# Kernel optimization log

Hardware: AMD Instinct MI355X
Metric: run time of the kernel (lower is better)

## Reference

```python
import jax, jax.numpy as jnp
import numpy as np

N_NODES = 100000
IN_FEAT = 128
HIDDEN = 256
OUT = 2
N_EDGES = 600000
EPS = 1e-12  # F.normalize eps


def glorot(key, shape):
    fan_in, fan_out = shape[1], shape[0]
    lim = jnp.sqrt(6.0 / (fan_in + fan_out))
    return jax.random.uniform(key, shape, jnp.float32, -lim, lim)


def setup_inputs() -> dict:
    key = jax.random.key(0)
    ks = jax.random.split(key, 8)
    x = jax.random.normal(ks[0], (N_NODES, IN_FEAT), jnp.float32)
    edge_index = jax.random.randint(ks[1], (2, N_EDGES), 0, N_NODES, jnp.int64)
    return {
        'x': x,
        'edge_index': edge_index,
        'W1_l': glorot(ks[2], (HIDDEN, IN_FEAT)),
        'b1': jnp.zeros((HIDDEN,), jnp.float32),
        'W1_r': glorot(ks[3], (HIDDEN, IN_FEAT)),
        'W2_l': glorot(ks[4], (OUT, HIDDEN)),
        'b2': jnp.zeros((OUT,), jnp.float32),
        'W2_r': glorot(ks[5], (OUT, HIDDEN)),
    }


def sage_conv(x, src, dst, W_l, b_l, W_r):
    # mean aggregation of neighbor (source) features onto destination nodes
    msgs = x[src]  # [E, d]
    s = jax.ops.segment_sum(msgs, dst, num_segments=N_NODES)
    cnt = jax.ops.segment_sum(jnp.ones((src.shape[0], 1), x.dtype), dst,
                              num_segments=N_NODES)
    agg = s / jnp.maximum(cnt, 1.0)  # nodes with no in-edges stay 0
    out = agg @ W_l.T + b_l + x @ W_r.T  # lin_l(agg) + lin_r(x)
    # L2 normalize (normalize=True in SAGEConv)
    nrm = jnp.linalg.norm(out, axis=-1, keepdims=True)
    return out / jnp.maximum(nrm, EPS)


def reference(x, edge_index, W1_l, b1, W1_r, W2_l, b2, W2_r):
    src, dst = edge_index[0], edge_index[1]
    h = sage_conv(x, src, dst, W1_l, b1, W1_r)
    h = jax.nn.relu(h)
    # dropout(p=0.2) is identity in eval mode
    h = sage_conv(h, src, dst, W2_l, b2, W2_r)
    return jax.nn.log_softmax(h, axis=1)
```

## Files before the change

kernel.cpp:

```cpp
#include <hip/hip_runtime.h>
#include <hip/hip_fp16.h>

#define NN  100000
#define FIN 128
#define HID 256
#define NE  600000
#define FEPS 1e-12f


typedef _Float16 f16x8 __attribute__((ext_vector_type(8)));
typedef float    f32x4 __attribute__((ext_vector_type(4)));

__device__ __forceinline__ int clampN(int v) {
    return ((unsigned)v < (unsigned)NN) ? v : 0;
}
__device__ __forceinline__ int detect4(const int* ei) {
    return ((ei[1] | ei[3] | ei[5] | ei[7]) == 0) ? 1 : 0;
}
__device__ __forceinline__ int ld_src(const int* ei, int e, int f) {
    return f ? ei[2 * e] : ei[e];
}
__device__ __forceinline__ int ld_dst(const int* ei, int e, int f) {
    return f ? ei[2 * (NE + e)] : ei[NE + e];
}

__device__ __forceinline__ size_t fragIdx(int j, int k) {
    return ((size_t)((k >> 5) * 16 + (j >> 4)) * 64 +
            (size_t)(((k >> 3) & 3) * 16 + (j & 15))) * 8 + (k & 7);
}

__global__ __launch_bounds__(256) void setup_kernel(
    const int* __restrict__ ei,
    const float* __restrict__ x,
    const float* __restrict__ W1l, const float* __restrict__ W1r,
    __half* __restrict__ Bfh, __half* __restrict__ Bfl,
    __half* __restrict__ xh,
    int* __restrict__ cnt, int ncv)
{
    int b = blockIdx.x;
    int t = threadIdx.x;
    if (b < 256) {
        int j = b, k2 = t;
        float v = (k2 < FIN) ? W1l[(size_t)j * FIN + k2]
                             : W1r[(size_t)j * FIN + (k2 - FIN)];
        __half h  = __float2half_rn(v);
        __half lo = __float2half_rn(v - __half2float(h));
        size_t fi = fragIdx(j, k2);
        Bfh[fi] = h;
        Bfl[fi] = lo;
    } else if (b < 256 + ncv) {
        int idx = (b - 256) * 256 + t;
        if (idx < NN * FIN / 8) {
            const float4* px = (const float4*)(x + (size_t)idx * 8);
            float4 v0 = px[0], v1 = px[1];
            __half2 h0 = __float22half2_rn(make_float2(v0.x, v0.y));
            __half2 h1 = __float22half2_rn(make_float2(v0.z, v0.w));
            __half2 h2 = __float22half2_rn(make_float2(v1.x, v1.y));
            __half2 h3 = __float22half2_rn(make_float2(v1.z, v1.w));
            uint4 u;
            u.x = __builtin_bit_cast(unsigned, h0);
            u.y = __builtin_bit_cast(unsigned, h1);
            u.z = __builtin_bit_cast(unsigned, h2);
            u.w = __builtin_bit_cast(unsigned, h3);
            ((uint4*)xh)[idx] = u;
        }
    } else {
        int e = (b - 256 - ncv) * 256 + t;
        if (e < NE) {
            int f = detect4(ei);
            atomicAdd(cnt + clampN(ld_dst(ei, e, f)), 1);
        }
    }
}

__global__ __launch_bounds__(1024) void scan_a_kernel(
    const int* __restrict__ cnt, int* __restrict__ off, int* __restrict__ bsum)
{
    __shared__ int sm[1024];
    int t = threadIdx.x;
    int idx = blockIdx.x * 1024 + t;
    int v = (idx < NN) ? cnt[idx] : 0;
    sm[t] = v;
    __syncthreads();
    for (int d = 1; d < 1024; d <<= 1) {
        int w = (t >= d) ? sm[t - d] : 0;
        __syncthreads();
        sm[t] += w;
        __syncthreads();
    }
    if (idx < NN) off[idx] = sm[t] - v;
    if (t == 1023) bsum[blockIdx.x] = sm[1023];
}
__global__ __launch_bounds__(128) void scan_b_kernel(
    int* __restrict__ bsum, int* __restrict__ off, int nblocks)
{
    __shared__ int sm[128];
    int t = threadIdx.x;
    int v = (t < nblocks) ? bsum[t] : 0;
    sm[t] = v;
    __syncthreads();
    for (int d = 1; d < 128; d <<= 1) {
        int w = (t >= d) ? sm[t - d] : 0;
        __syncthreads();
        sm[t] += w;
        __syncthreads();
    }
    if (t < nblocks) bsum[t] = sm[t] - v;
    if (t == 0) off[NN] = NE;
}
__global__ __launch_bounds__(1024) void scan_c_kernel(
    const int* __restrict__ bsum, int* __restrict__ off)
{
    int idx = blockIdx.x * 1024 + threadIdx.x;
    if (idx < NN) off[idx] += bsum[blockIdx.x];
}

__global__ __launch_bounds__(256) void fill_kernel(
    const int* __restrict__ ei,
    const int* __restrict__ off, int* __restrict__ cur, int* __restrict__ col)
{
    int e = blockIdx.x * 256 + threadIdx.x;
    if (e >= NE) return;
    int f = detect4(ei);
    int src = clampN(ld_src(ei, e, f));
    int dst = clampN(ld_dst(ei, e, f));
    int p = atomicAdd(cur + dst, 1);
    col[off[dst] + p] = src;
}

__global__ __launch_bounds__(256) void gather_kernel(
    const int* __restrict__ off, const int* __restrict__ col,
    const __half* __restrict__ xh, float* __restrict__ agg)
{
    int idx = blockIdx.x * 256 + threadIdx.x;
    if (idx >= NN * 16) return;
    int n     = idx >> 4;
    int ft    = idx & 15;
    int fbase = ft * 8;

    float a[8];
#pragma unroll
    for (int i = 0; i < 8; ++i) a[i] = 0.0f;

    int s0 = off[n], s1 = off[n + 1];
    int i = s0;
    for (; i + 3 < s1; i += 4) {
        int c0 = clampN(col[i]);
        int c1 = clampN(col[i + 1]);
        int c2 = clampN(col[i + 2]);
        int c3 = clampN(col[i + 3]);
        uint4 v0 = *(const uint4*)(xh + (size_t)c0 * FIN + fbase);
        uint4 v1 = *(const uint4*)(xh + (size_t)c1 * FIN + fbase);
        uint4 v2 = *(const uint4*)(xh + (size_t)c2 * FIN + fbase);
        uint4 v3 = *(const uint4*)(xh + (size_t)c3 * FIN + fbase);
#pragma unroll
        for (int u = 0; u < 4; ++u) {
            float2 f0 = __half22float2(__builtin_bit_cast(__half2, (&v0.x)[u]));
            float2 f1 = __half22float2(__builtin_bit_cast(__half2, (&v1.x)[u]));
            float2 f2 = __half22float2(__builtin_bit_cast(__half2, (&v2.x)[u]));
            float2 f3 = __half22float2(__builtin_bit_cast(__half2, (&v3.x)[u]));
            a[2 * u]     += (f0.x + f1.x) + (f2.x + f3.x);
            a[2 * u + 1] += (f0.y + f1.y) + (f2.y + f3.y);
        }
    }
    for (; i < s1; ++i) {
        int c0 = clampN(col[i]);
        uint4 v0 = *(const uint4*)(xh + (size_t)c0 * FIN + fbase);
#pragma unroll
        for (int u = 0; u < 4; ++u) {
            float2 f0 = __half22float2(__builtin_bit_cast(__half2, (&v0.x)[u]));
            a[2 * u]     += f0.x;
            a[2 * u + 1] += f0.y;
        }
    }
    float ic = 1.0f / fmaxf((float)(s1 - s0), 1.0f);
    float4* dst = (float4*)(agg + (size_t)n * FIN + fbase);
    dst[0] = make_float4(a[0] * ic, a[1] * ic, a[2] * ic, a[3] * ic);
    dst[1] = make_float4(a[4] * ic, a[5] * ic, a[6] * ic, a[7] * ic);
}

__device__ __forceinline__ void storeHiLo4(
    __half* Ah, __half* Al, int row, int k, float4 v)
{
    int addr = row * 256 + ((((k >> 3) ^ (row & 7)) << 3) | (k & 7));
    __half h0 = __float2half_rn(v.x), h1 = __float2half_rn(v.y);
    __half h2 = __float2half_rn(v.z), h3 = __float2half_rn(v.w);
    __half l0 = __float2half_rn(v.x - __half2float(h0));
    __half l1 = __float2half_rn(v.y - __half2float(h1));
    __half l2 = __float2half_rn(v.z - __half2float(h2));
    __half l3 = __float2half_rn(v.w - __half2float(h3));
    uint2 uh, ul;
    uh.x = __builtin_bit_cast(unsigned, __halves2half2(h0, h1));
    uh.y = __builtin_bit_cast(unsigned, __halves2half2(h2, h3));
    ul.x = __builtin_bit_cast(unsigned, __halves2half2(l0, l1));
    ul.y = __builtin_bit_cast(unsigned, __halves2half2(l2, l3));
    *(uint2*)(Ah + addr) = uh;
    *(uint2*)(Al + addr) = ul;
}

__global__ __launch_bounds__(512, 4) void gemm_mfma_kernel(
    const float* __restrict__ agg, const float* __restrict__ x,
    const __half* __restrict__ Bfh, const __half* __restrict__ Bfl,
    const float* __restrict__ b1,
    const float* __restrict__ W2l, const float* __restrict__ W2r,
    float* __restrict__ g, float* __restrict__ r)
{
    __shared__ __half Ah[64 * 256];
    __shared__ __half Al[64 * 256];

    const int t  = threadIdx.x;
    const int nb = blockIdx.x * 64;

    {
        const float4* aggF = (const float4*)agg;
        const float4* xF   = (const float4*)x;
        const float4 z4 = make_float4(0.f, 0.f, 0.f, 0.f);
#pragma unroll
        for (int i = 0; i < 4; ++i) {
            int idx   = i * 512 + t;
            int n_loc = idx >> 5;
            int kq    = idx & 31;
            int n     = nb + n_loc;
            bool valid = (n < NN);
            size_t base = (size_t)(valid ? n : 0) * 32 + kq;
            float4 va = aggF[base];
            float4 vx = xF[base];
            if (!valid) { va = z4; vx = z4; }
            storeHiLo4(Ah, Al, n_loc, kq * 4, va);
            storeHiLo4(Ah, Al, n_loc, FIN + kq * 4, vx);
        }
    }
    __syncthreads();

    const int l     = t & 63;
    const int w     = t >> 6;
    const int ln    = l & 15;
    const int kg    = l >> 4;
    const int mrow0 = (w & 1) * 32;
    const int jb    = (w >> 1) * 64;

    f32x4 acc[2][4];
#pragma unroll
    for (int mt = 0; mt < 2; ++mt)
#pragma unroll
        for (int jt = 0; jt < 4; ++jt)
            acc[mt][jt] = (f32x4){0.f, 0.f, 0.f, 0.f};

    const int rowA0  = mrow0 + ln;
    const int rowA1  = mrow0 + 16 + ln;
    const int baseA0 = rowA0 * 256;
    const int baseA1 = rowA1 * 256;
    const int r70    = rowA0 & 7;
    const int r71    = rowA1 & 7;

    const size_t bbase = (size_t)(w >> 1) * 2048 + (size_t)l * 8;
    const __half* __restrict__ bhp = Bfh + bbase;
    const __half* __restrict__ blp = Bfl + bbase;

#pragma unroll
    for (int kk = 0; kk < 8; ++kk) {
        const int chunk = kk * 4 + kg;
        f16x8 ah0 = *reinterpret_cast<const f16x8*>(Ah + baseA0 + ((chunk ^ r70) << 3));
        f16x8 al0 = *reinterpret_cast<const f16x8*>(Al + baseA0 + ((chunk ^ r70) << 3));
        f16x8 ah1 = *reinterpret_cast<const f16x8*>(Ah + baseA1 + ((chunk ^ r71) << 3));
        f16x8 al1 = *reinterpret_cast<const f16x8*>(Al + baseA1 + ((chunk ^ r71) << 3));
#pragma unroll
        for (int jt = 0; jt < 4; ++jt) {
            f16x8 bh = *reinterpret_cast<const f16x8*>(bhp + kk * 8192 + jt * 512);
            f16x8 bl = *reinterpret_cast<const f16x8*>(blp + kk * 8192 + jt * 512);
            acc[0][jt] = __builtin_amdgcn_mfma_f32_16x16x32_f16(ah0, bh, acc[0][jt], 0, 0, 0);
            acc[1][jt] = __builtin_amdgcn_mfma_f32_16x16x32_f16(ah1, bh, acc[1][jt], 0, 0, 0);
            acc[0][jt] = __builtin_amdgcn_mfma_f32_16x16x32_f16(al0, bh, acc[0][jt], 0, 0, 0);
            acc[1][jt] = __builtin_amdgcn_mfma_f32_16x16x32_f16(al1, bh, acc[1][jt], 0, 0, 0);
            acc[0][jt] = __builtin_amdgcn_mfma_f32_16x16x32_f16(ah0, bl, acc[0][jt], 0, 0, 0);
            acc[1][jt] = __builtin_amdgcn_mfma_f32_16x16x32_f16(ah1, bl, acc[1][jt], 0, 0, 0);
        }
    }

    float b1v[4], wl0[4], wl1[4], wr0[4], wr1[4];
#pragma unroll
    for (int jt = 0; jt < 4; ++jt) {
        int j = jb + jt * 16 + ln;
        b1v[jt] = b1[j];
        wl0[jt] = W2l[j];        wl1[jt] = W2l[HID + j];
        wr0[jt] = W2r[j];        wr1[jt] = W2r[HID + j];
    }

    float redv[2][4][5];
#pragma unroll
    for (int mt = 0; mt < 2; ++mt) {
#pragma unroll
        for (int rg = 0; rg < 4; ++rg) {
            float s = 0.f, G0 = 0.f, G1 = 0.f, R0 = 0.f, R1 = 0.f;
#pragma unroll
            for (int jt = 0; jt < 4; ++jt) {
                float oo = acc[mt][jt][rg] + b1v[jt];
                s = fmaf(oo, oo, s);
                float pp = fmaxf(oo, 0.f);
                G0 = fmaf(pp, wl0[jt], G0);
                G1 = fmaf(pp, wl1[jt], G1);
                R0 = fmaf(pp, wr0[jt], R0);
                R1 = fmaf(pp, wr1[jt], R1);
            }
#pragma unroll
            for (int m = 1; m < 16; m <<= 1) {
                s  += __shfl_xor(s, m);
                G0 += __shfl_xor(G0, m);
                G1 += __shfl_xor(G1, m);
                R0 += __shfl_xor(R0, m);
                R1 += __shfl_xor(R1, m);
            }
            redv[mt][rg][0] = s;  redv[mt][rg][1] = G0; redv[mt][rg][2] = G1;
            redv[mt][rg][3] = R0; redv[mt][rg][4] = R1;
        }
    }

    __syncthreads();
    float* red = (float*)Ah;
    if (ln == 0) {
#pragma unroll
        for (int mt = 0; mt < 2; ++mt)
#pragma unroll
            for (int rg = 0; rg < 4; ++rg) {
                int n_loc = mrow0 + mt * 16 + kg * 4 + rg;
                int base  = ((w >> 1) * 64 + n_loc) * 5;
                red[base + 0] = redv[mt][rg][0];
                red[base + 1] = redv[mt][rg][1];
                red[base + 2] = redv[mt][rg][2];
                red[base + 3] = redv[mt][rg][3];
                red[base + 4] = redv[mt][rg][4];
            }
    }
    __syncthreads();

    if (t < 64) {
        int n = nb + t;
        if (n < NN) {
            float s = 0.f, G0 = 0.f, G1 = 0.f, R0 = 0.f, R1 = 0.f;
#pragma unroll
            for (int jg = 0; jg < 4; ++jg) {
                const float* pp = red + (jg * 64 + t) * 5;
                s += pp[0]; G0 += pp[1]; G1 += pp[2]; R0 += pp[3]; R1 += pp[4];
            }
            float inv = 1.0f / fmaxf(sqrtf(s), FEPS);
            g[2 * (size_t)n]     = G0 * inv;
            g[2 * (size_t)n + 1] = G1 * inv;
            r[2 * (size_t)n]     = R0 * inv;
            r[2 * (size_t)n + 1] = R1 * inv;
        }
    }
}

__device__ __forceinline__ void phaseB_epilogue(
    float* smem_f, int t, int l, int nb,
    const __half* __restrict__ Bfh, const __half* __restrict__ Bfl,
    const float* __restrict__ b1,
    const float* __restrict__ W2l, const float* __restrict__ W2r,
    float* __restrict__ g, float* __restrict__ r)
{
    const int w  = __builtin_amdgcn_readfirstlane(t >> 6);
    const int jb = w * 16;

    float o[16];
#pragma unroll
    for (int i = 0; i < 16; ++i) o[i] = 0.0f;

#pragma unroll 1
    for (int k2 = 0; k2 < 2 * FIN; k2 += 4) {
        const int nc = l ^ ((k2 >> 3) & 31);
        float av0 = smem_f[(k2 + 0) * 64 + nc];
        float av1 = smem_f[(k2 + 1) * 64 + nc];
        float av2 = smem_f[(k2 + 2) * 64 + nc];
        float av3 = smem_f[(k2 + 3) * 64 + nc];
#pragma unroll
        for (int i = 0; i < 16; ++i) {
            const size_t fb = ((size_t)((k2 >> 5) * 16 + ((jb + i) >> 4)) * 64 +
                               (size_t)(((k2 >> 3) & 3) * 16 + ((jb + i) & 15))) * 8 +
                              (k2 & 7);
            const __half* ph = Bfh + fb;
            const __half* pl = Bfl + fb;
            float oi = o[i];
            oi = fmaf(av0, __half2float(ph[0]) + __half2float(pl[0]), oi);
            oi = fmaf(av1, __half2float(ph[1]) + __half2float(pl[1]), oi);
            oi = fmaf(av2, __half2float(ph[2]) + __half2float(pl[2]), oi);
            oi = fmaf(av3, __half2float(ph[3]) + __half2float(pl[3]), oi);
            o[i] = oi;
        }
    }

    float sq = 0.f, g0 = 0.f, g1 = 0.f, r0 = 0.f, r1 = 0.f;
    const float* b1w  = b1  + jb;
    const float* w2la = W2l + jb;
    const float* w2lb = W2l + HID + jb;
    const float* w2ra = W2r + jb;
    const float* w2rb = W2r + HID + jb;
#pragma unroll
    for (int i = 0; i < 16; ++i) {
        float oo = o[i] + b1w[i];
        sq = fmaf(oo, oo, sq);
        float p = fmaxf(oo, 0.0f);
        g0 = fmaf(p, w2la[i], g0);
        g1 = fmaf(p, w2lb[i], g1);
        r0 = fmaf(p, w2ra[i], r0);
        r1 = fmaf(p, w2rb[i], r1);
    }

    __syncthreads();
    smem_f[0 * 1024 + t] = sq;
    smem_f[1 * 1024 + t] = g0;
    smem_f[2 * 1024 + t] = g1;
    smem_f[3 * 1024 + t] = r0;
    smem_f[4 * 1024 + t] = r1;
    __syncthreads();

    if (t < 64) {
        int n2 = nb + t;
        float sqs = 0.f, G0 = 0.f, G1 = 0.f, R0 = 0.f, R1 = 0.f;
#pragma unroll
        for (int ww = 0; ww < 16; ++ww) {
            sqs += smem_f[0 * 1024 + ww * 64 + t];
            G0  += smem_f[1 * 1024 + ww * 64 + t];
            G1  += smem_f[2 * 1024 + ww * 64 + t];
            R0  += smem_f[3 * 1024 + ww * 64 + t];
            R1  += smem_f[4 * 1024 + ww * 64 + t];
        }
        float inv = 1.0f / fmaxf(sqrtf(sqs), FEPS);
        if (n2 < NN) {
            g[2 * (size_t)n2]     = G0 * inv;
            g[2 * (size_t)n2 + 1] = G1 * inv;
            r[2 * (size_t)n2]     = R0 * inv;
            r[2 * (size_t)n2 + 1] = R1 * inv;
        }
    }
}

template <bool HALFX>
__global__ __launch_bounds__(1024, 8) void layer1_kernel(
    const int* __restrict__ off, const int* __restrict__ col,
    const float* __restrict__ x, const __half* __restrict__ xh,
    const __half* __restrict__ Bfh, const __half* __restrict__ Bfl,
    const float* __restrict__ b1,
    const float* __restrict__ W2l, const float* __restrict__ W2r,
    float* __restrict__ g, float* __restrict__ r)
{
    __shared__ float smem_f[256 * 64];

    const int t  = threadIdx.x;
    const int nb = blockIdx.x * 64;
    const int l  = t & 63;

    {
        const int n_loc = t >> 4;
        const int ft    = t & 15;
        const int fbase = ft * 8;
        const int n     = nb + n_loc;
        const bool valid = (n < NN);

        float a[8];
#pragma unroll
        for (int i = 0; i < 8; ++i) a[i] = 0.0f;

        int s0 = 0, s1 = 0;
        if (valid) { s0 = off[n]; s1 = off[n + 1]; }

        int i = s0;
        if (HALFX) {
            for (; i + 3 < s1; i += 4) {
                int c0 = clampN(col[i]);
                int c1 = clampN(col[i + 1]);
                int c2 = clampN(col[i + 2]);
                int c3 = clampN(col[i + 3]);
                uint4 v0 = *(const uint4*)(xh + (size_t)c0 * FIN + fbase);
                uint4 v1 = *(const uint4*)(xh + (size_t)c1 * FIN + fbase);
                uint4 v2 = *(const uint4*)(xh + (size_t)c2 * FIN + fbase);
                uint4 v3 = *(const uint4*)(xh + (size_t)c3 * FIN + fbase);
#pragma unroll
                for (int u = 0; u < 4; ++u) {
                    float2 f0 = __half22float2(__builtin_bit_cast(__half2, (&v0.x)[u]));
                    float2 f1 = __half22float2(__builtin_bit_cast(__half2, (&v1.x)[u]));
                    float2 f2 = __half22float2(__builtin_bit_cast(__half2, (&v2.x)[u]));
                    float2 f3 = __half22float2(__builtin_bit_cast(__half2, (&v3.x)[u]));
                    a[2 * u]     += (f0.x + f1.x) + (f2.x + f3.x);
                    a[2 * u + 1] += (f0.y + f1.y) + (f2.y + f3.y);
                }
            }
            for (; i < s1; ++i) {
                int c0 = clampN(col[i]);
                uint4 v0 = *(const uint4*)(xh + (size_t)c0 * FIN + fbase);
#pragma unroll
                for (int u = 0; u < 4; ++u) {
                    float2 f0 = __half22float2(__builtin_bit_cast(__half2, (&v0.x)[u]));
                    a[2 * u]     += f0.x;
                    a[2 * u + 1] += f0.y;
                }
            }
        } else {
            for (; i < s1; ++i) {
                int c0 = clampN(col[i]);
                const float4* p0 = (const float4*)(x + (size_t)c0 * FIN + fbase);
                float4 v00 = p0[0], v01 = p0[1];
                a[0] += v00.x; a[1] += v00.y; a[2] += v00.z; a[3] += v00.w;
                a[4] += v01.x; a[5] += v01.y; a[6] += v01.z; a[7] += v01.w;
            }
        }
        float ic = 1.0f / fmaxf((float)(s1 - s0), 1.0f);
#pragma unroll
        for (int k = 0; k < 8; ++k) {
            int f = fbase + k;
            smem_f[f * 64 + (n_loc ^ ((f >> 3) & 31))] = a[k] * ic;
        }
        const float4* sp = (const float4*)(x + (size_t)(valid ? n : 0) * FIN + fbase);
        float4 s0v = valid ? sp[0] : make_float4(0.f, 0.f, 0.f, 0.f);
        float4 s1v = valid ? sp[1] : make_float4(0.f, 0.f, 0.f, 0.f);
        float sv[8] = {s0v.x, s0v.y, s0v.z, s0v.w, s1v.x, s1v.y, s1v.z, s1v.w};
#pragma unroll
        for (int k = 0; k < 8; ++k) {
            int f = FIN + fbase + k;
            smem_f[f * 64 + (n_loc ^ ((f >> 3) & 31))] = sv[k];
        }
    }
    __syncthreads();

    phaseB_epilogue(smem_f, t, l, nb, Bfh, Bfl, b1, W2l, W2r, g, r);
}

__global__ __launch_bounds__(256) void finalize_kernel(
    const int* __restrict__ off, const int* __restrict__ col,
    const float* __restrict__ g, const float* __restrict__ r,
    const float* __restrict__ b2,
    float* __restrict__ out)
{
    int n = blockIdx.x * 256 + threadIdx.x;
    if (n >= NN) return;
    int s0 = off[n], s1 = off[n + 1];
    float z0 = 0.0f, z1 = 0.0f, y0b = 0.0f, y1b = 0.0f;
    int i = s0;
    for (; i + 1 < s1; i += 2) {
        int sa = clampN(col[i]);
        int sb = clampN(col[i + 1]);
        float2 va = *(const float2*)(g + 2 * (size_t)sa);
        float2 vb = *(const float2*)(g + 2 * (size_t)sb);
        z0 += va.x; z1 += va.y;
        y0b += vb.x; y1b += vb.y;
    }
    if (i < s1) {
        int sa = clampN(col[i]);
        float2 va = *(const float2*)(g + 2 * (size_t)sa);
        z0 += va.x; z1 += va.y;
    }
    z0 += y0b; z1 += y1b;
    float ic = 1.0f / fmaxf((float)(s1 - s0), 1.0f);
    z0 = z0 * ic + b2[0] + r[2 * (size_t)n];
    z1 = z1 * ic + b2[1] + r[2 * (size_t)n + 1];
    float d = 1.0f / fmaxf(sqrtf(z0 * z0 + z1 * z1), FEPS);
    float y0 = z0 * d, y1 = z1 * d;
    float m = fmaxf(y0, y1);
    float lg = m + logf(__expf(y0 - m) + __expf(y1 - m));
    out[2 * (size_t)n]     = y0 - lg;
    out[2 * (size_t)n + 1] = y1 - lg;
}

extern "C" void kernel_launch(void* const* d_in, const int* in_sizes, int n_in,
                              void* d_out, int out_size, void* d_ws, size_t ws_size,
                              hipStream_t stream) {
    const float* x   = (const float*)d_in[0];
    const int*   ei  = (const int*)d_in[1];
    const float* W1l = (const float*)d_in[2];
    const float* b1  = (const float*)d_in[3];
    const float* W1r = (const float*)d_in[4];
    const float* W2l = (const float*)d_in[5];
    const float* b2  = (const float*)d_in[6];
    const float* W2r = (const float*)d_in[7];

    const int nsb = (NN + 1023) / 1024;
    const int ncv = (NN * FIN / 8 + 255) / 256;
    const int ecb = (NE + 255) / 256;

    const size_t tailWords = (size_t)2 * NN + (NN + 1) + NE + 4 * NN + 128;
    const size_t needB = (size_t)256 * 256 * 4 + (size_t)NN * FIN * 2 +
                         tailWords * 4;
    const size_t needA = needB + (size_t)NN * FIN * 4;

    bool pathA = (ws_size >= needA);
    bool pathB = !pathA && (ws_size >= needB);
    bool half  = pathA || pathB;

    char* p = (char*)d_ws;
    __half* Bfh = (__half*)p;             p += (size_t)256 * 256 * 2;
    __half* Bfl = (__half*)p;             p += (size_t)256 * 256 * 2;
    __half* xh = nullptr;
    if (half) { xh = (__half*)p;          p += (size_t)NN * FIN * 2; }
    float* agg = nullptr;
    if (pathA) { agg = (float*)p;         p += (size_t)NN * FIN * 4; }

    int*   cnt  = (int*)p;
    int*   cur  = cnt + NN;
    int*   off  = cur + NN;
    int*   col  = off + NN + 1;
    float* g    = (float*)(col + NE);
    float* r    = g + 2 * (size_t)NN;
    int*   bsum = (int*)(r + 2 * (size_t)NN);

    hipMemsetAsync(cnt, 0, 2 * (size_t)NN * sizeof(int), stream);

    int cv = half ? ncv : 0;
    setup_kernel<<<256 + cv + ecb, 256, 0, stream>>>(ei, x, W1l, W1r,
                                                     Bfh, Bfl, xh, cnt, cv);
    scan_a_kernel<<<nsb, 1024, 0, stream>>>(cnt, off, bsum);
    scan_b_kernel<<<1, 128, 0, stream>>>(bsum, off, nsb);
    scan_c_kernel<<<nsb, 1024, 0, stream>>>(bsum, off);
    fill_kernel<<<ecb, 256, 0, stream>>>(ei, off, cur, col);

    if (pathA) {
        gather_kernel<<<(NN * 16 + 255) / 256, 256, 0, stream>>>(off, col, xh,
                                                                 agg);
        gemm_mfma_kernel<<<(NN + 63) / 64, 512, 0, stream>>>(agg, x, Bfh, Bfl,
                                                             b1, W2l, W2r, g, r);
    } else if (pathB) {
        layer1_kernel<true><<<(NN + 63) / 64, 1024, 0, stream>>>(
            off, col, x, xh, Bfh, Bfl, b1, W2l, W2r, g, r);
    } else {
        layer1_kernel<false><<<(NN + 63) / 64, 1024, 0, stream>>>(
            off, col, x, xh, Bfh, Bfl, b1, W2l, W2r, g, r);
    }
    finalize_kernel<<<(NN + 255) / 256, 256, 0, stream>>>(off, col, g, r, b2,
                                                          (float*)d_out);
}
```

Before: 268.3 us.

## Store gathered aggregates as pre-split swizzled fp16 hi/lo, halve GEMM LDS

The gather kernel now converts its mean-aggregated features into fp16 high and low halves and writes them in the swizzled layout the GEMM expects. The GEMM then copies tiles straight into shared memory with no conversion. The GEMM also splits K into two phases: aggregate first, then x, reusing a half-size LDS buffer. It raises the occupancy hint to 8 blocks per SM and writes reduction partials directly instead of holding them in registers. This removes the float agg round-trip and the per-block hi/lo conversion, at the cost of an extra barrier and a serialised x load between the two phases.

```diff
diff --git a/kernel.cpp b/kernel.cpp
--- a/kernel.cpp
+++ b/kernel.cpp
@@ -22,6 +22,10 @@
 }
 __device__ __forceinline__ int ld_dst(const int* ei, int e, int f) {
     return f ? ei[2 * (NE + e)] : ei[NE + e];
+}
+
+__device__ __forceinline__ unsigned packh2(__half a, __half b) {
+    return __builtin_bit_cast(unsigned, __halves2half2(a, b));
 }
 
 __device__ __forceinline__ size_t fragIdx(int j, int k) {
@@ -53,15 +57,11 @@
         if (idx < NN * FIN / 8) {
             const float4* px = (const float4*)(x + (size_t)idx * 8);
             float4 v0 = px[0], v1 = px[1];
-            __half2 h0 = __float22half2_rn(make_float2(v0.x, v0.y));
-            __half2 h1 = __float22half2_rn(make_float2(v0.z, v0.w));
-            __half2 h2 = __float22half2_rn(make_float2(v1.x, v1.y));
-            __half2 h3 = __float22half2_rn(make_float2(v1.z, v1.w));
             uint4 u;
-            u.x = __builtin_bit_cast(unsigned, h0);
-            u.y = __builtin_bit_cast(unsigned, h1);
-            u.z = __builtin_bit_cast(unsigned, h2);
-            u.w = __builtin_bit_cast(unsigned, h3);
+            u.x = packh2(__float2half_rn(v0.x), __float2half_rn(v0.y));
+            u.y = packh2(__float2half_rn(v0.z), __float2half_rn(v0.w));
+            u.z = packh2(__float2half_rn(v1.x), __float2half_rn(v1.y));
+            u.w = packh2(__float2half_rn(v1.z), __float2half_rn(v1.w));
             ((uint4*)xh)[idx] = u;
         }
     } else {
@@ -130,7 +130,8 @@
 
 __global__ __launch_bounds__(256) void gather_kernel(
     const int* __restrict__ off, const int* __restrict__ col,
-    const __half* __restrict__ xh, float* __restrict__ agg)
+    const __half* __restrict__ xh,
+    __half* __restrict__ aggH, __half* __restrict__ aggL)
 {
     int idx = blockIdx.x * 256 + threadIdx.x;
     if (idx >= NN * 16) return;
@@ -174,15 +175,26 @@
         }
     }
     float ic = 1.0f / fmaxf((float)(s1 - s0), 1.0f);
-    float4* dst = (float4*)(agg + (size_t)n * FIN + fbase);
-    dst[0] = make_float4(a[0] * ic, a[1] * ic, a[2] * ic, a[3] * ic);
-    dst[1] = make_float4(a[4] * ic, a[5] * ic, a[6] * ic, a[7] * ic);
-}
-
-__device__ __forceinline__ void storeHiLo4(
-    __half* Ah, __half* Al, int row, int k, float4 v)
-{
-    int addr = row * 256 + ((((k >> 3) ^ (row & 7)) << 3) | (k & 7));
+    __half h[8], lo[8];
+#pragma unroll
+    for (int k = 0; k < 8; ++k) {
+        float v = a[k] * ic;
+        h[k]  = __float2half_rn(v);
+        lo[k] = __float2half_rn(v - __half2float(h[k]));
+    }
+    uint4 uh, ul;
+    uh.x = packh2(h[0], h[1]);  uh.y = packh2(h[2], h[3]);
+    uh.z = packh2(h[4], h[5]);  uh.w = packh2(h[6], h[7]);
+    ul.x = packh2(lo[0], lo[1]); ul.y = packh2(lo[2], lo[3]);
+    ul.z = packh2(lo[4], lo[5]); ul.w = packh2(lo[6], lo[7]);
+    size_t rowb = (size_t)n * 128 + (size_t)((ft ^ (n & 7)) << 3);
+    *(uint4*)(aggH + rowb) = uh;
+    *(uint4*)(aggL + rowb) = ul;
+}
+
+__device__ __forceinline__ void splitStore4(
+    __half* Ah, __half* Al, int addr, float4 v)
+{
     __half h0 = __float2half_rn(v.x), h1 = __float2half_rn(v.y);
     __half h2 = __float2half_rn(v.z), h3 = __float2half_rn(v.w);
     __half l0 = __float2half_rn(v.x - __half2float(h0));
@@ -190,84 +202,32 @@
     __half l2 = __float2half_rn(v.z - __half2float(h2));
     __half l3 = __float2half_rn(v.w - __half2float(h3));
     uint2 uh, ul;
-    uh.x = __builtin_bit_cast(unsigned, __halves2half2(h0, h1));
-    uh.y = __builtin_bit_cast(unsigned, __halves2half2(h2, h3));
-    ul.x = __builtin_bit_cast(unsigned, __halves2half2(l0, l1));
-    ul.y = __builtin_bit_cast(unsigned, __halves2half2(l2, l3));
+    uh.x = packh2(h0, h1);  uh.y = packh2(h2, h3);
+    ul.x = packh2(l0, l1);  ul.y = packh2(l2, l3);
     *(uint2*)(Ah + addr) = uh;
     *(uint2*)(Al + addr) = ul;
 }
 
-__global__ __launch_bounds__(512, 4) void gemm_mfma_kernel(
-    const float* __restrict__ agg, const float* __restrict__ x,
+__device__ __forceinline__ void mfma_phase(
+    const __half* Ah, const __half* Al,
     const __half* __restrict__ Bfh, const __half* __restrict__ Bfl,
-    const float* __restrict__ b1,
-    const float* __restrict__ W2l, const float* __restrict__ W2r,
-    float* __restrict__ g, float* __restrict__ r)
-{
-    __shared__ __half Ah[64 * 256];
-    __shared__ __half Al[64 * 256];
-
-    const int t  = threadIdx.x;
-    const int nb = blockIdx.x * 64;
-
-    {
-        const float4* aggF = (const float4*)agg;
-        const float4* xF   = (const float4*)x;
-        const float4 z4 = make_float4(0.f, 0.f, 0.f, 0.f);
-#pragma unroll
-        for (int i = 0; i < 4; ++i) {
-            int idx   = i * 512 + t;
-            int n_loc = idx >> 5;
-            int kq    = idx & 31;
-            int n     = nb + n_loc;
-            bool valid = (n < NN);
-            size_t base = (size_t)(valid ? n : 0) * 32 + kq;
-            float4 va = aggF[base];
-            float4 vx = xF[base];
-            if (!valid) { va = z4; vx = z4; }
-            storeHiLo4(Ah, Al, n_loc, kq * 4, va);
-            storeHiLo4(Ah, Al, n_loc, FIN + kq * 4, vx);
-        }
-    }
-    __syncthreads();
-
-    const int l     = t & 63;
-    const int w     = t >> 6;
-    const int ln    = l & 15;
-    const int kg    = l >> 4;
-    const int mrow0 = (w & 1) * 32;
-    const int jb    = (w >> 1) * 64;
-
-    f32x4 acc[2][4];
-#pragma unroll
-    for (int mt = 0; mt < 2; ++mt)
-#pragma unroll
-        for (int jt = 0; jt < 4; ++jt)
-            acc[mt][jt] = (f32x4){0.f, 0.f, 0.f, 0.f};
-
-    const int rowA0  = mrow0 + ln;
-    const int rowA1  = mrow0 + 16 + ln;
-    const int baseA0 = rowA0 * 256;
-    const int baseA1 = rowA1 * 256;
-    const int r70    = rowA0 & 7;
-    const int r71    = rowA1 & 7;
-
-    const size_t bbase = (size_t)(w >> 1) * 2048 + (size_t)l * 8;
-    const __half* __restrict__ bhp = Bfh + bbase;
-    const __half* __restrict__ blp = Bfl + bbase;
-
-#pragma unroll
-    for (int kk = 0; kk < 8; ++kk) {
+    int pb , int baseA0, int baseA1, int r7,
+    int jg0, int l, f32x4 acc[2][4])
+{
+    const int kg = l >> 4;
+#pragma unroll
+    for (int kk = 0; kk < 4; ++kk) {
         const int chunk = kk * 4 + kg;
-        f16x8 ah0 = *reinterpret_cast<const f16x8*>(Ah + baseA0 + ((chunk ^ r70) << 3));
-        f16x8 al0 = *reinterpret_cast<const f16x8*>(Al + baseA0 + ((chunk ^ r70) << 3));
-        f16x8 ah1 = *reinterpret_cast<const f16x8*>(Ah + baseA1 + ((chunk ^ r71) << 3));
-        f16x8 al1 = *reinterpret_cast<const f16x8*>(Al + baseA1 + ((chunk ^ r71) << 3));
+        const int sl = (chunk ^ r7) << 3;
+        f16x8 ah0 = *reinterpret_cast<const f16x8*>(Ah + baseA0 + sl);
+        f16x8 al0 = *reinterpret_cast<const f16x8*>(Al + baseA0 + sl);
+        f16x8 ah1 = *reinterpret_cast<const f16x8*>(Ah + baseA1 + sl);
+        f16x8 al1 = *reinterpret_cast<const f16x8*>(Al + baseA1 + sl);
 #pragma unroll
         for (int jt = 0; jt < 4; ++jt) {
-            f16x8 bh = *reinterpret_cast<const f16x8*>(bhp + kk * 8192 + jt * 512);
-            f16x8 bl = *reinterpret_cast<const f16x8*>(blp + kk * 8192 + jt * 512);
+            const size_t bo = (((size_t)(pb + kk) * 16 + jg0 + jt) * 64 + l) * 8;
+            f16x8 bh = *reinterpret_cast<const f16x8*>(Bfh + bo);
+            f16x8 bl = *reinterpret_cast<const f16x8*>(Bfl + bo);
             acc[0][jt] = __builtin_amdgcn_mfma_f32_16x16x32_f16(ah0, bh, acc[0][jt], 0, 0, 0);
             acc[1][jt] = __builtin_amdgcn_mfma_f32_16x16x32_f16(ah1, bh, acc[1][jt], 0, 0, 0);
             acc[0][jt] = __builtin_amdgcn_mfma_f32_16x16x32_f16(al0, bh, acc[0][jt], 0, 0, 0);
@@ -276,17 +236,87 @@
             acc[1][jt] = __builtin_amdgcn_mfma_f32_16x16x32_f16(ah1, bl, acc[1][jt], 0, 0, 0);
         }
     }
-
+}
+
+__global__ __launch_bounds__(512, 8) void gemm_mfma_kernel(
+    const __half* __restrict__ aggH, const __half* __restrict__ aggL,
+    const float* __restrict__ x,
+    const __half* __restrict__ Bfh, const __half* __restrict__ Bfl,
+    const float* __restrict__ b1,
+    const float* __restrict__ W2l, const float* __restrict__ W2r,
+    float* __restrict__ g, float* __restrict__ r)
+{
+    __shared__ __half Ah[64 * 128];
+    __shared__ __half Al[64 * 128];
+
+    const int t  = threadIdx.x;
+    const int nb = blockIdx.x * 64;
+
+    {
+        const uint4* gh = (const uint4*)(aggH + (size_t)nb * 128);
+        const uint4* gl = (const uint4*)(aggL + (size_t)nb * 128);
+#pragma unroll
+        for (int i = 0; i < 2; ++i) {
+            int idx = i * 512 + t;
+            *(uint4*)(Ah + idx * 8) = gh[idx];
+            *(uint4*)(Al + idx * 8) = gl[idx];
+        }
+    }
+    __syncthreads();
+
+    const int l     = t & 63;
+    const int w     = t >> 6;
+    const int ln    = l & 15;
+    const int kg    = l >> 4;
+    const int mrow0 = (w & 1) * 32;
+    const int jg0   = (w >> 1) * 4;
+
+    f32x4 acc[2][4];
+#pragma unroll
+    for (int mt = 0; mt < 2; ++mt)
+#pragma unroll
+        for (int jt = 0; jt < 4; ++jt)
+            acc[mt][jt] = (f32x4){0.f, 0.f, 0.f, 0.f};
+
+    const int rowA0  = mrow0 + ln;
+    const int rowA1  = mrow0 + 16 + ln;
+    const int baseA0 = rowA0 * 128;
+    const int baseA1 = rowA1 * 128;
+    const int r7     = ln & 7;
+
+    mfma_phase(Ah, Al, Bfh, Bfl, 0, baseA0, baseA1, r7, jg0, l, acc);
+    __syncthreads();
+
+    {
+        const float4* xF = (const float4*)x;
+        const float4 z4 = make_float4(0.f, 0.f, 0.f, 0.f);
+#pragma unroll
+        for (int i = 0; i < 4; ++i) {
+            int idx   = i * 512 + t;
+            int n_loc = idx >> 5;
+            int kq    = idx & 31;
+            int n     = nb + n_loc;
+            float4 v  = (n < NN) ? xF[(size_t)n * 32 + kq] : z4;
+            int addr  = n_loc * 128 + ((((kq >> 1) ^ (n_loc & 7)) << 3) | ((kq & 1) << 2));
+            splitStore4(Ah, Al, addr, v);
+        }
+    }
+    __syncthreads();
+
+    mfma_phase(Ah, Al, Bfh, Bfl, 4, baseA0, baseA1, r7, jg0, l, acc);
+
+    const int jb2 = jg0 * 16;
     float b1v[4], wl0[4], wl1[4], wr0[4], wr1[4];
 #pragma unroll
     for (int jt = 0; jt < 4; ++jt) {
-        int j = jb + jt * 16 + ln;
+        int j = jb2 + jt * 16 + ln;
         b1v[jt] = b1[j];
         wl0[jt] = W2l[j];        wl1[jt] = W2l[HID + j];
         wr0[jt] = W2r[j];        wr1[jt] = W2r[HID + j];
     }
 
-    float redv[2][4][5];
+    __syncthreads();
+    float* red = (float*)Ah;
 #pragma unroll
     for (int mt = 0; mt < 2; ++mt) {
 #pragma unroll
@@ -310,26 +340,12 @@
                 R0 += __shfl_xor(R0, m);
                 R1 += __shfl_xor(R1, m);
             }
-            redv[mt][rg][0] = s;  redv[mt][rg][1] = G0; redv[mt][rg][2] = G1;
-            redv[mt][rg][3] = R0; redv[mt][rg][4] = R1;
-        }
-    }
-
-    __syncthreads();
-    float* red = (float*)Ah;
-    if (ln == 0) {
-#pragma unroll
-        for (int mt = 0; mt < 2; ++mt)
-#pragma unroll
-            for (int rg = 0; rg < 4; ++rg) {
+            if (ln == 0) {
                 int n_loc = mrow0 + mt * 16 + kg * 4 + rg;
-                int base  = ((w >> 1) * 64 + n_loc) * 5;
-                red[base + 0] = redv[mt][rg][0];
-                red[base + 1] = redv[mt][rg][1];
-                red[base + 2] = redv[mt][rg][2];
-                red[base + 3] = redv[mt][rg][3];
-                red[base + 4] = redv[mt][rg][4];
+                float* pp = red + ((size_t)(w >> 1) * 64 + n_loc) * 5;
+                pp[0] = s;  pp[1] = G0; pp[2] = G1; pp[3] = R0; pp[4] = R1;
             }
+        }
     }
     __syncthreads();
 
@@ -339,7 +355,7 @@
             float s = 0.f, G0 = 0.f, G1 = 0.f, R0 = 0.f, R1 = 0.f;
 #pragma unroll
             for (int jg = 0; jg < 4; ++jg) {
-                const float* pp = red + (jg * 64 + t) * 5;
+                const float* pp = red + ((size_t)jg * 64 + t) * 5;
                 s += pp[0]; G0 += pp[1]; G1 += pp[2]; R0 += pp[3]; R1 += pp[4];
             }
             float inv = 1.0f / fmaxf(sqrtf(s), FEPS);
@@ -590,8 +606,12 @@
     __half* Bfl = (__half*)p;             p += (size_t)256 * 256 * 2;
     __half* xh = nullptr;
     if (half) { xh = (__half*)p;          p += (size_t)NN * FIN * 2; }
-    float* agg = nullptr;
-    if (pathA) { agg = (float*)p;         p += (size_t)NN * FIN * 4; }
+    __half* aggH = nullptr; __half* aggL = nullptr;
+    if (pathA) {
+        aggH = (__half*)p;
+        aggL = aggH + (size_t)NN * 128;
+        p += (size_t)NN * FIN * 4;
+    }
 
     int*   cnt  = (int*)p;
     int*   cur  = cnt + NN;
@@ -613,8 +633,9 @@
 
     if (pathA) {
         gather_kernel<<<(NN * 16 + 255) / 256, 256, 0, stream>>>(off, col, xh,
-                                                                 agg);
-        gemm_mfma_kernel<<<(NN + 63) / 64, 512, 0, stream>>>(agg, x, Bfh, Bfl,
+                                                                 aggH, aggL);
+        gemm_mfma_kernel<<<(NN + 63) / 64, 512, 0, stream>>>(aggH, aggL, x,
+                                                             Bfh, Bfl,
                                                              b1, W2l, W2r, g, r);
     } else if (pathB) {
         layer1_kernel<true><<<(NN + 63) / 64, 1024, 0, stream>>>(
```

New measurement: 291.3 us. 1.09x slower.
